# Kernel tuning notes

Hardware: AMD Instinct MI355X
Metric: run time of the kernel (lower is better)

Reference implementation:

```python
import jax, jax.numpy as jnp
import numpy as np

N_NODES = 50000
N_EDGES = 800000
D = 64
N_BASIS = 8


def setup_inputs() -> dict:
    key = jax.random.key(0)
    ks = jax.random.split(key, 16)
    inp = {
        "p": jax.random.normal(ks[0], (N_NODES, D), dtype=jnp.float32),
        "idx_i": jax.random.randint(ks[1], (N_EDGES,), 0, N_NODES),
        "idx_j": jax.random.randint(ks[2], (N_EDGES,), 0, N_NODES),
        "basis": jax.random.normal(ks[3], (N_EDGES, N_BASIS), dtype=jnp.float32),
        # pp_layer MLP: [64, 64, 64], activation tanh between layers
        "pp_W1": jax.random.normal(ks[4], (D, D), dtype=jnp.float32) / np.sqrt(D),
        "pp_b1": jnp.zeros((D,), dtype=jnp.float32),
        "pp_W2": jax.random.normal(ks[5], (D, D), dtype=jnp.float32) / np.sqrt(D),
        "pp_b2": jnp.zeros((D,), dtype=jnp.float32),
        # pi_layer MLP: n_neurons = [128, 64, 64, 64*8], activation=None, last layer no bias
        "pi_W1": jax.random.normal(ks[6], (2 * D, D), dtype=jnp.float32) / np.sqrt(2 * D),
        "pi_b1": jnp.zeros((D,), dtype=jnp.float32),
        "pi_W2": jax.random.normal(ks[7], (D, D), dtype=jnp.float32) / np.sqrt(D),
        "pi_b2": jnp.zeros((D,), dtype=jnp.float32),
        "pi_W3": jax.random.normal(ks[8], (D, D * N_BASIS), dtype=jnp.float32) / np.sqrt(D),
        # ii_layer MLP: [64, 64, 64], activation tanh between layers
        "ii_W1": jax.random.normal(ks[9], (D, D), dtype=jnp.float32) / np.sqrt(D),
        "ii_b1": jnp.zeros((D,), dtype=jnp.float32),
        "ii_W2": jax.random.normal(ks[10], (D, D), dtype=jnp.float32) / np.sqrt(D),
        "ii_b2": jnp.zeros((D,), dtype=jnp.float32),
    }
    return inp


def reference(p, idx_i, idx_j, basis,
              pp_W1, pp_b1, pp_W2, pp_b2,
              pi_W1, pi_b1, pi_W2, pi_b2, pi_W3,
              ii_W1, ii_b1, ii_W2, ii_b2):
    # pp_layer: node MLP (tanh between layers, no activation after last)
    p1 = jnp.tanh(p @ pp_W1 + pp_b1) @ pp_W2 + pp_b2          # [N, D]

    # PILayer: gather endpoint features, concat, linear MLP (activation=None), basis contraction
    inter = jnp.concatenate([p1[idx_i], p1[idx_j]], axis=-1)  # [E, 2D]
    inter = inter @ pi_W1 + pi_b1                              # [E, D]
    inter = inter @ pi_W2 + pi_b2                              # [E, D]
    inter = inter @ pi_W3                                      # [E, D*n_basis] (no bias)
    inter = inter.reshape(inter.shape[0], D, N_BASIS)          # [E, D, n_basis]
    i1 = jnp.einsum('ecb,eb->ec', inter, basis)                # [E, D]

    # ii_layer: edge MLP
    i1 = jnp.tanh(i1 @ ii_W1 + ii_b1) @ ii_W2 + ii_b2          # [E, D]

    # IPLayer: scatter_add edge features back to nodes (dim_size = p1.shape[0])
    out = jax.ops.segment_sum(i1, idx_j, num_segments=p1.shape[0])  # [N, D]
    return out
```

## Files before the change

### kernel.cpp

```cpp
#include <hip/hip_runtime.h>

#define N_NODES 50000
#define N_EDGES 800000

typedef float f32x4 __attribute__((ext_vector_type(4)));
typedef short bf16x8 __attribute__((ext_vector_type(8)));

__device__ __forceinline__ float fast_tanh(float x) {
  float e = __expf(2.0f * x);
  return 1.0f - 2.0f / (e + 1.0f);
}

__device__ __forceinline__ unsigned short f2bf_rne(float x) {
  unsigned u = __float_as_uint(x);
  unsigned r = u + 0x7FFFu + ((u >> 16) & 1u);
  return (unsigned short)(r >> 16);
}

__global__ __launch_bounds__(256) void prep1_kernel(
    const float* __restrict__ piW1, const float* __restrict__ pib1,
    const float* __restrict__ piW2, const float* __restrict__ pib2,
    float* __restrict__ W12, float* __restrict__ b12) {
  int gid = blockIdx.x * 256 + threadIdx.x;
  if (gid < 128 * 64) {
    int m = gid >> 6, c = gid & 63;
    float acc = 0.f;
    #pragma unroll 8
    for (int k = 0; k < 64; ++k) acc = fmaf(piW1[m * 64 + k], piW2[k * 64 + c], acc);
    W12[gid] = acc;
  } else if (gid < 128 * 64 + 64) {
    int c = gid - 128 * 64;
    float acc = pib2[c];
    for (int k = 0; k < 64; ++k) acc = fmaf(pib1[k], piW2[k * 64 + c], acc);
    b12[c] = acc;
  }
}

__global__ __launch_bounds__(256) void prep_b_kernel(
    const float* __restrict__ piW3, const float* __restrict__ iiW1,
    unsigned short* __restrict__ Bpack) {
  int gid = blockIdx.x * 256 + threadIdx.x;
  int j = gid & 7;
  int lane = (gid >> 3) & 63;
  int ct = (gid >> 9) & 3;
  int ks = gid >> 11;
  int kidx = ks * 32 + ((lane >> 4) << 3) + j;
  int col = ct * 16 + (lane & 15);
  int k = kidx >> 3, b = kidx & 7;
  float acc = 0.f;
  #pragma unroll 8
  for (int mm = 0; mm < 64; ++mm)
    acc = fmaf(piW3[k * 512 + mm * 8 + b], iiW1[mm * 64 + col], acc);
  Bpack[gid] = f2bf_rne(acc);
}

__global__ __launch_bounds__(256) void prep_w2_kernel(
    const float* __restrict__ iiW2, unsigned short* __restrict__ W2pack) {
  int gid = blockIdx.x * 256 + threadIdx.x;
  int j = gid & 7;
  int lane = (gid >> 3) & 63;
  int ct = (gid >> 9) & 3;
  int ks = gid >> 11;
  int kidx = ks * 32 + ((lane >> 4) << 3) + j;
  int col = ct * 16 + (lane & 15);
  W2pack[gid] = f2bf_rne(iiW2[kidx * 64 + col]);
}

__global__ __launch_bounds__(256) void node_kernel(
    const float* __restrict__ p,
    const float* __restrict__ ppW1, const float* __restrict__ ppb1,
    const float* __restrict__ ppW2, const float* __restrict__ ppb2,
    const float* __restrict__ W12,
    float* __restrict__ qa, float* __restrict__ qb) {
  __shared__ float sW1[64 * 64];
  __shared__ float sW2[64 * 64];
  __shared__ float sW12[128 * 64];
  __shared__ float sb1[64], sb2[64];
  __shared__ float sX[4][8][64];
  int tid = threadIdx.x;
  for (int i = tid; i < 64 * 64; i += 256) { sW1[i] = ppW1[i]; sW2[i] = ppW2[i]; }
  for (int i = tid; i < 128 * 64; i += 256) sW12[i] = W12[i];
  if (tid < 64) { sb1[tid] = ppb1[tid]; sb2[tid] = ppb2[tid]; }
  __syncthreads();
  int wave = tid >> 6, lane = tid & 63;
  int rowbase = blockIdx.x * 32 + wave * 8;

  float4* sXf4 = (float4*)&sX[wave][0][0];
  for (int t = lane; t < 128; t += 64) {
    int r = t >> 4, c4 = t & 15;
    int row = rowbase + r;
    float4 v = make_float4(0.f, 0.f, 0.f, 0.f);
    if (row < N_NODES) v = ((const float4*)p)[row * 16 + c4];
    sXf4[t] = v;
  }
  __syncthreads();

  float h[8];
  #pragma unroll
  for (int r = 0; r < 8; ++r) h[r] = sb1[lane];
  for (int k = 0; k < 64; ++k) {
    float w = sW1[k * 64 + lane];
    #pragma unroll
    for (int r = 0; r < 8; ++r) h[r] = fmaf(sX[wave][r][k], w, h[r]);
  }
  #pragma unroll
  for (int r = 0; r < 8; ++r) h[r] = fast_tanh(h[r]);
  __syncthreads();
  #pragma unroll
  for (int r = 0; r < 8; ++r) sX[wave][r][lane] = h[r];
  __syncthreads();

  float g[8];
  #pragma unroll
  for (int r = 0; r < 8; ++r) g[r] = sb2[lane];
  for (int k = 0; k < 64; ++k) {
    float w = sW2[k * 64 + lane];
    #pragma unroll
    for (int r = 0; r < 8; ++r) g[r] = fmaf(sX[wave][r][k], w, g[r]);
  }
  __syncthreads();
  #pragma unroll
  for (int r = 0; r < 8; ++r) sX[wave][r][lane] = g[r];
  __syncthreads();

  float a[8], b[8];
  #pragma unroll
  for (int r = 0; r < 8; ++r) { a[r] = 0.f; b[r] = 0.f; }
  for (int k = 0; k < 64; ++k) {
    float wa = sW12[k * 64 + lane];
    float wb = sW12[(64 + k) * 64 + lane];
    #pragma unroll
    for (int r = 0; r < 8; ++r) {
      float x = sX[wave][r][k];
      a[r] = fmaf(x, wa, a[r]);
      b[r] = fmaf(x, wb, b[r]);
    }
  }
  #pragma unroll
  for (int r = 0; r < 8; ++r) {
    int row = rowbase + r;
    if (row < N_NODES) {
      qa[row * 64 + lane] = a[r];
      qb[row * 64 + lane] = b[r];
    }
  }
}

__global__ __launch_bounds__(1024, 8) void edge_kernel(
    const int* __restrict__ idx_i, const int* __restrict__ idx_j,
    const float* __restrict__ basis,
    const float* __restrict__ qa, const float* __restrict__ qb,
    const float* __restrict__ b12,
    const unsigned short* __restrict__ Bpack,
    const unsigned short* __restrict__ W2pack,
    const float* __restrict__ iib1, const float* __restrict__ iib2,
    float* __restrict__ out) {
  __shared__ __align__(16) unsigned short sB[32768];
  float* sH2 = (float*)sB;
  unsigned short* sT = sB;

  int tid = threadIdx.x;
  int e0 = blockIdx.x * 256;

  for (int t = tid; t < 4096; t += 1024) {
    int e = t >> 4, q = t & 15;
    int ii = idx_i[e0 + e];
    int jj = idx_j[e0 + e];
    float4 va = ((const float4*)qa)[ii * 16 + q];
    float4 vb = ((const float4*)qb)[jj * 16 + q];
    float4 vc = ((const float4*)b12)[q];
    float4 h;
    h.x = va.x + vb.x + vc.x;
    h.y = va.y + vb.y + vc.y;
    h.z = va.z + vb.z + vc.z;
    h.w = va.w + vb.w + vc.w;
    int dw = e * 64 + ((q * 4) ^ ((e & 7) << 3));
    *((float4*)(sH2 + dw)) = h;
  }
  __syncthreads();

  int w = tid >> 6, l = tid & 63;
  int m = l & 15, s = l >> 4;
  int eloc = w * 16 + m;
  int swz = (eloc & 7) << 3;

  float h2r[16];
  #pragma unroll
  for (int t = 0; t < 16; ++t) h2r[t] = sH2[eloc * 64 + ((t * 4 + s) ^ swz)];

  float bas[8];
  {
    const float4* bp = (const float4*)(basis + (size_t)(e0 + eloc) * 8);
    float4 b0 = bp[0], b1 = bp[1];
    bas[0] = b0.x; bas[1] = b0.y; bas[2] = b0.z; bas[3] = b0.w;
    bas[4] = b1.x; bas[5] = b1.y; bas[6] = b1.z; bas[7] = b1.w;
  }
  __syncthreads();

  {
    const uint4* g = (const uint4*)Bpack;
    uint4* d = (uint4*)sB;
    #pragma unroll
    for (int t = 0; t < 4; ++t) d[tid + t * 1024] = g[tid + t * 1024];
  }
  __syncthreads();

  f32x4 c0, c1, c2, c3;
  {
    float v0 = iib1[m], v1 = iib1[16 + m], v2 = iib1[32 + m], v3 = iib1[48 + m];
    c0 = (f32x4){v0, v0, v0, v0};
    c1 = (f32x4){v1, v1, v1, v1};
    c2 = (f32x4){v2, v2, v2, v2};
    c3 = (f32x4){v3, v3, v3, v3};
  }

  const bf16x8* Bl = (const bf16x8*)sB;
  #pragma unroll
  for (int ks = 0; ks < 16; ++ks) {
    bf16x8 B0 = Bl[(ks * 4 + 0) * 64 + l];
    bf16x8 B1 = Bl[(ks * 4 + 1) * 64 + l];
    bf16x8 B2 = Bl[(ks * 4 + 2) * 64 + l];
    bf16x8 B3 = Bl[(ks * 4 + 3) * 64 + l];
    float hv = h2r[ks];
    union { unsigned u[4]; bf16x8 v; } A;
    #pragma unroll
    for (int j = 0; j < 4; ++j) {
      float p0 = hv * bas[2 * j];
      float p1 = hv * bas[2 * j + 1];
      asm("v_cvt_pk_bf16_f32 %0, %1, %2" : "=v"(A.u[j]) : "v"(p0), "v"(p1));
    }
    c0 = __builtin_amdgcn_mfma_f32_16x16x32_bf16(A.v, B0, c0, 0, 0, 0);
    c1 = __builtin_amdgcn_mfma_f32_16x16x32_bf16(A.v, B1, c1, 0, 0, 0);
    c2 = __builtin_amdgcn_mfma_f32_16x16x32_bf16(A.v, B2, c2, 0, 0, 0);
    c3 = __builtin_amdgcn_mfma_f32_16x16x32_bf16(A.v, B3, c3, 0, 0, 0);
  }
  __syncthreads();

  #pragma unroll
  for (int r = 0; r < 4; ++r) {
    int row = w * 16 + s * 4 + r;
    sT[row * 72 + 0 * 16 + m] = f2bf_rne(fast_tanh(c0[r]));
    sT[row * 72 + 1 * 16 + m] = f2bf_rne(fast_tanh(c1[r]));
    sT[row * 72 + 2 * 16 + m] = f2bf_rne(fast_tanh(c2[r]));
    sT[row * 72 + 3 * 16 + m] = f2bf_rne(fast_tanh(c3[r]));
  }
  __syncthreads();

  f32x4 d0, d1, d2, d3;
  {
    float v0 = iib2[m], v1 = iib2[16 + m], v2 = iib2[32 + m], v3 = iib2[48 + m];
    d0 = (f32x4){v0, v0, v0, v0};
    d1 = (f32x4){v1, v1, v1, v1};
    d2 = (f32x4){v2, v2, v2, v2};
    d3 = (f32x4){v3, v3, v3, v3};
  }
  const bf16x8* Wl = (const bf16x8*)W2pack;
  #pragma unroll
  for (int ks = 0; ks < 2; ++ks) {
    bf16x8 Af = *(const bf16x8*)(sT + eloc * 72 + ks * 32 + s * 8);
    d0 = __builtin_amdgcn_mfma_f32_16x16x32_bf16(Af, Wl[(ks * 4 + 0) * 64 + l], d0, 0, 0, 0);
    d1 = __builtin_amdgcn_mfma_f32_16x16x32_bf16(Af, Wl[(ks * 4 + 1) * 64 + l], d1, 0, 0, 0);
    d2 = __builtin_amdgcn_mfma_f32_16x16x32_bf16(Af, Wl[(ks * 4 + 2) * 64 + l], d2, 0, 0, 0);
    d3 = __builtin_amdgcn_mfma_f32_16x16x32_bf16(Af, Wl[(ks * 4 + 3) * 64 + l], d3, 0, 0, 0);
  }

  #pragma unroll
  for (int r = 0; r < 4; ++r) {
    int jj = idx_j[e0 + w * 16 + s * 4 + r];
    float* po = out + (size_t)jj * 64;
    atomicAdd(po + m, d0[r]);
    atomicAdd(po + 16 + m, d1[r]);
    atomicAdd(po + 32 + m, d2[r]);
    atomicAdd(po + 48 + m, d3[r]);
  }
}

extern "C" void kernel_launch(void* const* d_in, const int* in_sizes, int n_in,
                              void* d_out, int out_size, void* d_ws, size_t ws_size,
                              hipStream_t stream) {
  const float* p     = (const float*)d_in[0];
  const int*   idx_i = (const int*)d_in[1];
  const int*   idx_j = (const int*)d_in[2];
  const float* basis = (const float*)d_in[3];
  const float* ppW1  = (const float*)d_in[4];
  const float* ppb1  = (const float*)d_in[5];
  const float* ppW2  = (const float*)d_in[6];
  const float* ppb2  = (const float*)d_in[7];
  const float* piW1  = (const float*)d_in[8];
  const float* pib1  = (const float*)d_in[9];
  const float* piW2  = (const float*)d_in[10];
  const float* pib2  = (const float*)d_in[11];
  const float* piW3  = (const float*)d_in[12];
  const float* iiW1  = (const float*)d_in[13];
  const float* iib1  = (const float*)d_in[14];
  const float* iiW2  = (const float*)d_in[15];
  const float* iib2  = (const float*)d_in[16];

  float* ws  = (float*)d_ws;
  float* qa  = ws;
  float* qb  = ws + 3200000;
  float* W12 = ws + 6400000;
  float* b12 = ws + 6408192;
  unsigned short* Bpack  = (unsigned short*)(ws + 6408256);
  unsigned short* W2pack = (unsigned short*)(ws + 6408256 + 16384);

  hipMemsetAsync(d_out, 0, (size_t)out_size * sizeof(float), stream);
  prep1_kernel<<<33, 256, 0, stream>>>(piW1, pib1, piW2, pib2, W12, b12);
  prep_b_kernel<<<128, 256, 0, stream>>>(piW3, iiW1, Bpack);
  prep_w2_kernel<<<16, 256, 0, stream>>>(iiW2, W2pack);
  node_kernel<<<1563, 256, 0, stream>>>(p, ppW1, ppb1, ppW2, ppb2, W12, qa, qb);
  edge_kernel<<<3125, 1024, 0, stream>>>(idx_i, idx_j, basis, qa, qb, b12,
                                         Bpack, W2pack, iib1, iib2, (float*)d_out);
}
```

Measured before the change: 300.5 us.

## Counting-sort edges by destination and pre-reduce runs before atomic scatter

Adds a histogram, a single-block prefix scan and a scatter kernel that sort edges by destination node, and the edge kernel now reads the sorted index arrays. After the MLPs, results are staged in shared memory and consecutive edges with the same destination are summed before one atomicAdd per run, which is meant to cut global atomic traffic. In exchange there are three extra kernels with their own atomics, a serial single-block scan, and basis rows now read through an indirection.

Result: slower. 393.8 us (+31.0%).

```diff
diff --git a/kernel.cpp b/kernel.cpp
--- a/kernel.cpp
+++ b/kernel.cpp
@@ -2,6 +2,7 @@
 
 #define N_NODES 50000
 #define N_EDGES 800000
+#define NPAD 50176
 
 typedef float f32x4 __attribute__((ext_vector_type(4)));
 typedef short bf16x8 __attribute__((ext_vector_type(8)));
@@ -66,6 +67,52 @@
   W2pack[gid] = f2bf_rne(iiW2[kidx * 64 + col]);
 }
 
+__global__ __launch_bounds__(256) void hist_kernel(
+    const int* __restrict__ idx_j, int* __restrict__ counts) {
+  int e = blockIdx.x * 256 + threadIdx.x;
+  if (e < N_EDGES) atomicAdd(&counts[idx_j[e]], 1);
+}
+
+__global__ __launch_bounds__(1024) void scan_kernel(
+    const int* __restrict__ counts, int* __restrict__ offsets,
+    int* __restrict__ cursors) {
+  __shared__ int buf[1024];
+  int tid = threadIdx.x;
+  int base = 0;
+  for (int c = 0; c < NPAD / 1024; ++c) {
+    int idx = c * 1024 + tid;
+    int v = counts[idx];
+    buf[tid] = v;
+    __syncthreads();
+    for (int off = 1; off < 1024; off <<= 1) {
+      int t = (tid >= off) ? buf[tid - off] : 0;
+      __syncthreads();
+      buf[tid] += t;
+      __syncthreads();
+    }
+    int excl = buf[tid] - v;
+    offsets[idx] = base + excl;
+    cursors[idx] = base + excl;
+    base += buf[1023];
+    __syncthreads();
+  }
+}
+
+__global__ __launch_bounds__(256) void sort_scatter_kernel(
+    const int* __restrict__ idx_i, const int* __restrict__ idx_j,
+    int* __restrict__ cursors,
+    int* __restrict__ sorted_i, int* __restrict__ sorted_j,
+    int* __restrict__ sorted_e) {
+  int e = blockIdx.x * 256 + threadIdx.x;
+  if (e < N_EDGES) {
+    int j = idx_j[e];
+    int pos = atomicAdd(&cursors[j], 1);
+    sorted_i[pos] = idx_i[e];
+    sorted_j[pos] = j;
+    sorted_e[pos] = e;
+  }
+}
+
 __global__ __launch_bounds__(256) void node_kernel(
     const float* __restrict__ p,
     const float* __restrict__ ppW1, const float* __restrict__ ppb1,
@@ -147,7 +194,8 @@
 }
 
 __global__ __launch_bounds__(1024, 8) void edge_kernel(
-    const int* __restrict__ idx_i, const int* __restrict__ idx_j,
+    const int* __restrict__ sorted_i, const int* __restrict__ sorted_j,
+    const int* __restrict__ sorted_e,
     const float* __restrict__ basis,
     const float* __restrict__ qa, const float* __restrict__ qb,
     const float* __restrict__ b12,
@@ -158,14 +206,15 @@
   __shared__ __align__(16) unsigned short sB[32768];
   float* sH2 = (float*)sB;
   unsigned short* sT = sB;
+  float* sF = (float*)sB;
 
   int tid = threadIdx.x;
   int e0 = blockIdx.x * 256;
 
   for (int t = tid; t < 4096; t += 1024) {
     int e = t >> 4, q = t & 15;
-    int ii = idx_i[e0 + e];
-    int jj = idx_j[e0 + e];
+    int ii = sorted_i[e0 + e];
+    int jj = sorted_j[e0 + e];
     float4 va = ((const float4*)qa)[ii * 16 + q];
     float4 vb = ((const float4*)qb)[jj * 16 + q];
     float4 vc = ((const float4*)b12)[q];
@@ -190,7 +239,8 @@
 
   float bas[8];
   {
-    const float4* bp = (const float4*)(basis + (size_t)(e0 + eloc) * 8);
+    int eorig = sorted_e[e0 + eloc];
+    const float4* bp = (const float4*)(basis + (size_t)eorig * 8);
     float4 b0 = bp[0], b1 = bp[1];
     bas[0] = b0.x; bas[1] = b0.y; bas[2] = b0.z; bas[3] = b0.w;
     bas[4] = b1.x; bas[5] = b1.y; bas[6] = b1.z; bas[7] = b1.w;
@@ -265,13 +315,38 @@
   }
 
   #pragma unroll
-  for (int r = 0; r < 4; ++r) {
-    int jj = idx_j[e0 + w * 16 + s * 4 + r];
-    float* po = out + (size_t)jj * 64;
-    atomicAdd(po + m, d0[r]);
-    atomicAdd(po + 16 + m, d1[r]);
-    atomicAdd(po + 32 + m, d2[r]);
-    atomicAdd(po + 48 + m, d3[r]);
+  for (int h = 0; h < 2; ++h) {
+    __syncthreads();
+    if ((w >> 3) == h) {
+      int wl = w & 7;
+      #pragma unroll
+      for (int r = 0; r < 4; ++r) {
+        int row = wl * 16 + s * 4 + r;
+        sF[row * 68 + 0  + m] = d0[r];
+        sF[row * 68 + 16 + m] = d1[r];
+        sF[row * 68 + 32 + m] = d2[r];
+        sF[row * 68 + 48 + m] = d3[r];
+      }
+    }
+    __syncthreads();
+    {
+      int base_e = e0 + h * 128 + w * 8;
+      float acc = sF[(w * 8) * 68 + l];
+      int cur_j = sorted_j[base_e];
+      #pragma unroll
+      for (int rr = 1; rr < 8; ++rr) {
+        int nj = sorted_j[base_e + rr];
+        float v = sF[(w * 8 + rr) * 68 + l];
+        if (nj == cur_j) {
+          acc += v;
+        } else {
+          atomicAdd(&out[(size_t)cur_j * 64 + l], acc);
+          acc = v;
+          cur_j = nj;
+        }
+      }
+      atomicAdd(&out[(size_t)cur_j * 64 + l], acc);
+    }
   }
 }
 
@@ -302,13 +377,25 @@
   float* W12 = ws + 6400000;
   float* b12 = ws + 6408192;
   unsigned short* Bpack  = (unsigned short*)(ws + 6408256);
-  unsigned short* W2pack = (unsigned short*)(ws + 6408256 + 16384);
+  unsigned short* W2pack = (unsigned short*)(ws + 6424640);
+  int* counts   = (int*)(ws + 6426688);
+  int* offsets  = (int*)(ws + 6476864);
+  int* cursors  = (int*)(ws + 6527040);
+  int* sorted_i = (int*)(ws + 6577216);
+  int* sorted_j = (int*)(ws + 7377216);
+  int* sorted_e = (int*)(ws + 8177216);
 
   hipMemsetAsync(d_out, 0, (size_t)out_size * sizeof(float), stream);
+  hipMemsetAsync(counts, 0, (size_t)NPAD * sizeof(int), stream);
   prep1_kernel<<<33, 256, 0, stream>>>(piW1, pib1, piW2, pib2, W12, b12);
   prep_b_kernel<<<128, 256, 0, stream>>>(piW3, iiW1, Bpack);
   prep_w2_kernel<<<16, 256, 0, stream>>>(iiW2, W2pack);
+  hist_kernel<<<3125, 256, 0, stream>>>(idx_j, counts);
+  scan_kernel<<<1, 1024, 0, stream>>>(counts, offsets, cursors);
+  sort_scatter_kernel<<<3125, 256, 0, stream>>>(idx_i, idx_j, cursors,
+                                                sorted_i, sorted_j, sorted_e);
   node_kernel<<<1563, 256, 0, stream>>>(p, ppW1, ppb1, ppW2, ppb2, W12, qa, qb);
-  edge_kernel<<<3125, 1024, 0, stream>>>(idx_i, idx_j, basis, qa, qb, b12,
-                                         Bpack, W2pack, iib1, iib2, (float*)d_out);
-}
+  edge_kernel<<<3125, 1024, 0, stream>>>(sorted_i, sorted_j, sorted_e, basis,
+                                         qa, qb, b12, Bpack, W2pack,
+                                         iib1, iib2, (float*)d_out);
+}
```
